# Optimization experiments

Hardware: AMD Instinct MI355X
Metric: run time of the kernel (lower is better)

The kernel has to match this reference:

```python
import jax, jax.numpy as jnp
import numpy as np

N_NODES = 100000
N_EDGES = 1600000
HID = 128
HEADS = 8
DK = HID // HEADS
N_LAYERS = 4
IN_DIM = 32
N_CLASSES = 16


def _ln(x, g, b, eps=1e-5):
    mu = x.mean(-1, keepdims=True)
    var = x.var(-1, keepdims=True)
    return (x - mu) / jnp.sqrt(var + eps) * g + b


def setup_inputs() -> dict:
    key = jax.random.key(0)
    ks = jax.random.split(key, 24)
    s = 0.05
    inp = {
        'feat': jax.random.randint(ks[0], (N_NODES,), 0, IN_DIM, dtype=jnp.int32),
        'edge_src': jax.random.randint(ks[1], (N_EDGES,), 0, N_NODES, dtype=jnp.int32),
        'edge_dst': jnp.sort(jax.random.randint(ks[2], (N_EDGES,), 0, N_NODES, dtype=jnp.int32)),
        'emb': jax.random.normal(ks[3], (IN_DIM, HID), jnp.float32) * s,
        'Wq': jax.random.normal(ks[4], (N_LAYERS, HID, HID), jnp.float32) * s,
        'Wk': jax.random.normal(ks[5], (N_LAYERS, HID, HID), jnp.float32) * s,
        'Wv': jax.random.normal(ks[6], (N_LAYERS, HID, HID), jnp.float32) * s,
        'Wo': jax.random.normal(ks[7], (N_LAYERS, HID, HID), jnp.float32) * s,
        'bo': jnp.zeros((N_LAYERS, HID), jnp.float32),
        'ln1_g': jnp.ones((N_LAYERS, HID), jnp.float32),
        'ln1_b': jnp.zeros((N_LAYERS, HID), jnp.float32),
        'W1': jax.random.normal(ks[8], (N_LAYERS, HID, 2 * HID), jnp.float32) * s,
        'b1': jnp.zeros((N_LAYERS, 2 * HID), jnp.float32),
        'W2': jax.random.normal(ks[9], (N_LAYERS, 2 * HID, HID), jnp.float32) * s,
        'b2': jnp.zeros((N_LAYERS, HID), jnp.float32),
        'ln2_g': jnp.ones((N_LAYERS, HID), jnp.float32),
        'ln2_b': jnp.zeros((N_LAYERS, HID), jnp.float32),
        'mW0': jax.random.normal(ks[10], (HID, HID // 2), jnp.float32) * s,
        'mb0': jnp.zeros((HID // 2,), jnp.float32),
        'mW1': jax.random.normal(ks[11], (HID // 2, HID // 4), jnp.float32) * s,
        'mb1': jnp.zeros((HID // 4,), jnp.float32),
        'mW2': jax.random.normal(ks[12], (HID // 4, N_CLASSES), jnp.float32) * s,
        'mb2': jnp.zeros((N_CLASSES,), jnp.float32),
    }
    return inp


def reference(feat, edge_src, edge_dst, emb, Wq, Wk, Wv, Wo, bo, ln1_g, ln1_b,
              W1, b1, W2, b2, ln2_g, ln2_b, mW0, mb0, mW1, mb1, mW2, mb2):
    N = feat.shape[0]
    h = emb[feat]  # [N, HID] embedding gather
    inv_sqrt_dk = jnp.float32(1.0 / np.sqrt(DK))
    for l in range(Wq.shape[0]):
        h_in1 = h
        q = (h @ Wq[l]).reshape(N, HEADS, DK)
        k = (h @ Wk[l]).reshape(N, HEADS, DK)
        v = (h @ Wv[l]).reshape(N, HEADS, DK)
        # per-edge scores: K[src] . Q[dst], scaled, clipped, exponentiated
        sc = jnp.einsum('ehd,ehd->eh', k[edge_src], q[edge_dst]) * inv_sqrt_dk
        sc = jnp.exp(jnp.clip(sc, -5.0, 5.0))  # [E, HEADS]
        wV = jax.ops.segment_sum(sc[:, :, None] * v[edge_src], edge_dst, num_segments=N)
        z = jax.ops.segment_sum(sc, edge_dst, num_segments=N)
        attn = (wV / (z[:, :, None] + 1e-6)).reshape(N, HID)
        h = h_in1 + (attn @ Wo[l] + bo[l])  # residual + O proj
        h = _ln(h, ln1_g[l], ln1_b[l])
        h_in2 = h
        f = jax.nn.relu(h @ W1[l] + b1[l]) @ W2[l] + b2[l]
        h = _ln(h_in2 + f, ln2_g[l], ln2_b[l])
    # MLPReadout: HID -> HID/2 -> HID/4 -> n_classes
    h = jax.nn.relu(h @ mW0 + mb0)
    h = jax.nn.relu(h @ mW1 + mb1)
    return h @ mW2 + mb2
```

## Files before the change

### kernel.cpp

```cpp
#include <hip/hip_runtime.h>
#include <hip/hip_fp16.h>

#define HID 128
#define N_LAYERS 4
#define IN_DIM 32
#define N_CLASSES 16

typedef _Float16 f16x8 __attribute__((ext_vector_type(8)));
typedef _Float16 half2_t __attribute__((ext_vector_type(2)));
typedef float f32x2 __attribute__((ext_vector_type(2)));
typedef __attribute__((ext_vector_type(4))) float f32x4;
typedef unsigned int uint_t;

#if defined(__has_builtin)
#if __has_builtin(__builtin_amdgcn_cvt_pk_f32_fp8)
#define HAVE_CVT_FP8 1
#endif
#if __has_builtin(__builtin_amdgcn_cvt_pk_fp8_f32)
#define HAVE_ENC_FP8 1
#endif
#endif

__device__ __forceinline__ unsigned short f2bf(float f) {
    unsigned int u = __float_as_uint(f);
    return (unsigned short)((u + 0x7FFFu + ((u >> 16) & 1u)) >> 16);
}
__device__ __forceinline__ float2 up16(uint_t u) {
    __half2 h = *(__half2*)&u;
    return __half22float2(h);
}

__device__ __forceinline__ unsigned char f2e4m3(float f) {
    unsigned int u = __float_as_uint(f);
    unsigned char s = (unsigned char)((u >> 24) & 0x80u);
    unsigned int a = u & 0x7FFFFFFFu;
    if (a >= 0x43E00000u) return s | 0x7Eu;
    int exp = (int)(a >> 23) - 127;
    if (exp < -6) {
        int m = (int)rintf(__uint_as_float(a) * 512.f);
        return s | (unsigned char)m;
    }
    unsigned int lsb = (a >> 20) & 1u;
    a += 0x7FFFFu + lsb;
    int e8 = ((int)(a >> 23) - 127) + 7;
    unsigned int m8 = (a >> 20) & 7u;
    return s | (unsigned char)((e8 << 3) | (int)m8);
}
__device__ __forceinline__ float e4m32f(unsigned int b) {
    unsigned int s = (b & 0x80u) << 24;
    unsigned int E = (b >> 3) & 15u, m = b & 7u;
    if (E == 0) {
        float v = (float)m * 0.001953125f;
        return __uint_as_float(__float_as_uint(v) | s);
    }
    return __uint_as_float(s | ((E + 120u) << 23) | (m << 20));
}
__device__ __forceinline__ unsigned char enc8(float v) {
#ifdef HAVE_ENC_FP8
    int r = __builtin_amdgcn_cvt_pk_fp8_f32(v, v, 0, false);
    return (unsigned char)(r & 0xFF);
#else
    return f2e4m3(v);
#endif
}
__device__ __forceinline__ void dec8v(uint_t u, f32x2* o) {
#ifdef HAVE_CVT_FP8
    o[0] = __builtin_amdgcn_cvt_pk_f32_fp8(u, false);
    o[1] = __builtin_amdgcn_cvt_pk_f32_fp8(u, true);
#else
    o[0] = (f32x2){e4m32f(u & 255u), e4m32f((u >> 8) & 255u)};
    o[1] = (f32x2){e4m32f((u >> 16) & 255u), e4m32f(u >> 24)};
#endif
}

__global__ void detect_kernel(const unsigned int* __restrict__ ln1g, int* __restrict__ flag) {
    if (threadIdx.x == 0 && blockIdx.x == 0)
        *flag = (ln1g[0] == 0x3F800000u) ? 0 : 1;
}

#define NSM 11
struct SArgs {
    const void* src[NSM];
    float*      dst[NSM];
    int         cnt[NSM];
};

__global__ void conv_kernel(SArgs args, const int* __restrict__ flag) {
    int p = blockIdx.y;
    int n = args.cnt[p];
    int base = (blockIdx.x * 256 + threadIdx.x) * 4;
    if (base >= n) return;
    float* dst = args.dst[p];
    if (*flag) {
        const unsigned short* s = (const unsigned short*)args.src[p];
        #pragma unroll
        for (int j = 0; j < 4; ++j)
            dst[base + j] = __uint_as_float(((unsigned int)s[base + j]) << 16);
    } else {
        const float* s = (const float*)args.src[p];
        *(float4*)&dst[base] = *(const float4*)&s[base];
    }
}

#define NW 27
struct WArgs {
    const void* src[NW];
    int         soff[NW];
    _Float16*   dst[NW];
    int         K[NW];
    int         M[NW];
};

__global__ void wconv_kernel(WArgs a, const int* __restrict__ flag) {
    int p = blockIdx.y;
    int K = a.K[p], M = a.M[p];
    int idx = blockIdx.x * 256 + threadIdx.x;
    if (idx >= K * M) return;
    int k = idx / M, m = idx % M;
    float v;
    if (*flag)
        v = __uint_as_float(((unsigned int)((const unsigned short*)a.src[p])[a.soff[p] + idx]) << 16);
    else
        v = ((const float*)a.src[p])[a.soff[p] + idx];
    a.dst[p][(size_t)m * K + k] = (_Float16)v;
}

__global__ void csr_kernel(const int* __restrict__ dst, int* __restrict__ row_start,
                           int N, int E) {
    int n = blockIdx.x * 256 + threadIdx.x;
    if (n > N) return;
    int lo = 0, hi = E;
    while (lo < hi) {
        int mid = (lo + hi) >> 1;
        if (dst[mid] < n) lo = mid + 1; else hi = mid;
    }
    row_start[n] = lo;
}

__global__ void embed_kernel(const int* __restrict__ feat, const float* __restrict__ emb,
                             _Float16* __restrict__ h, int N) {
    int idx = blockIdx.x * 256 + threadIdx.x;
    if (idx >= N * 16) return;
    int n  = idx >> 4;
    int c8 = idx & 15;
    int f = feat[n];
    const float* s = &emb[(size_t)f * HID + c8 * 8];
    float4 a = *(const float4*)s;
    float4 b = *(const float4*)(s + 4);
    f16x8 o;
    o[0] = (_Float16)a.x; o[1] = (_Float16)a.y; o[2] = (_Float16)a.z; o[3] = (_Float16)a.w;
    o[4] = (_Float16)b.x; o[5] = (_Float16)b.y; o[6] = (_Float16)b.z; o[7] = (_Float16)b.w;
    *(f16x8*)&h[(size_t)n * HID + c8 * 8] = o;
}

template<int K, int KC, int MC, int MTOT, bool RELU, bool BIAS, int OUTMODE>
__launch_bounds__(256)
__global__ void mfma_gemm(const _Float16* __restrict__ Ain,
                          const _Float16* __restrict__ Bt,
                          const float* __restrict__ bias,
                          float* __restrict__ Cf, _Float16* __restrict__ C16,
                          _Float16* __restrict__ q16, unsigned char* __restrict__ kvp8,
                          void* __restrict__ outp, const int* __restrict__ flag, int Nrow) {
    constexpr int NT  = MC / 16;
    constexpr int SAB = KC * 2 + 16;
    constexpr int KNC = K / KC;

    __shared__ __align__(16) char As[64 * SAB];
    __shared__ __align__(16) char Bs[MC * SAB];

    const int t    = threadIdx.x;
    const int w    = t >> 6;
    const int l    = t & 63;
    const int quad = l >> 4;
    const int lc   = l & 15;
    const int row0 = blockIdx.x * 64;
    const int mbase = blockIdx.y * MC;

    f32x4 acc[NT];
    #pragma unroll
    for (int i = 0; i < NT; ++i) acc[i] = (f32x4){0.f, 0.f, 0.f, 0.f};

    for (int kc0 = 0; kc0 < K; kc0 += KC) {
        if (KNC > 1 && kc0 > 0) __syncthreads();
        constexpr int AU = 64 * KC / 8;
        #pragma unroll
        for (int i = 0; i < (AU + 255) / 256; ++i) {
            int idx = t + i * 256;
            if ((AU % 256 == 0) || idx < AU) {
                int r = idx / (KC / 8), u = idx % (KC / 8);
                *(uint4*)&As[r * SAB + u * 16] =
                    *(const uint4*)(Ain + (size_t)(row0 + r) * K + kc0 + u * 8);
            }
        }
        constexpr int BU = MC * KC / 8;
        #pragma unroll
        for (int i = 0; i < (BU + 255) / 256; ++i) {
            int idx = t + i * 256;
            if ((BU % 256 == 0) || idx < BU) {
                int m = idx / (KC / 8), u = idx % (KC / 8);
                *(uint4*)&Bs[m * SAB + u * 16] =
                    *(const uint4*)(Bt + (size_t)(mbase + m) * K + kc0 + u * 8);
            }
        }
        __syncthreads();
        #pragma unroll
        for (int kk = 0; kk < KC / 32; ++kk) {
            f16x8 af = *(const f16x8*)&As[(w * 16 + lc) * SAB + kk * 64 + quad * 16];
            #pragma unroll
            for (int i = 0; i < NT; ++i) {
                f16x8 bf = *(const f16x8*)&Bs[(i * 16 + lc) * SAB + kk * 64 + quad * 16];
                acc[i] = __builtin_amdgcn_mfma_f32_16x16x32_f16(af, bf, acc[i], 0, 0, 0);
            }
        }
    }

    if (BIAS) {
        #pragma unroll
        for (int i = 0; i < NT; ++i) {
            float bv = bias[mbase + i * 16 + lc];
            #pragma unroll
            for (int r = 0; r < 4; ++r) acc[i][r] += bv;
        }
    }
    #pragma unroll
    for (int r = 0; r < 4; ++r) {
        int row = row0 + w * 16 + quad * 4 + r;
        #pragma unroll
        for (int i = 0; i < NT; ++i) {
            float v = acc[i][r];
            if (RELU) v = fmaxf(v, 0.f);
            if (OUTMODE == 0) {
                Cf[(size_t)row * MTOT + mbase + i * 16 + lc] = v;
            } else if (OUTMODE == 1) {
                C16[(size_t)row * MTOT + mbase + i * 16 + lc] = (_Float16)v;
            } else if (OUTMODE == 2) {
                int gc = mbase + i * 16 + lc;
                if (gc < 128)      q16[(size_t)row * 128 + gc] = (_Float16)v;
                else if (gc < 256) kvp8[(size_t)row * 256 + (gc - 128)] = enc8(v);
                else               kvp8[(size_t)row * 256 + 128 + (gc - 256)] = enc8(v);
            } else {
                if (row < Nrow) {
                    size_t o = (size_t)row * MTOT + mbase + i * 16 + lc;
                    if (*flag) ((unsigned short*)outp)[o] = f2bf(v);
                    else       ((float*)outp)[o] = v;
                }
            }
        }
    }
}

__launch_bounds__(256)
__global__ void layer_tail(const _Float16* __restrict__ t2, _Float16* __restrict__ h,
                           const _Float16* __restrict__ Wo, const _Float16* __restrict__ W1,
                           const _Float16* __restrict__ W2,
                           const float* __restrict__ bo,  const float* __restrict__ l1g,
                           const float* __restrict__ l1b, const float* __restrict__ b1,
                           const float* __restrict__ b2,  const float* __restrict__ l2g,
                           const float* __restrict__ l2b) {
    constexpr int SAB = 272;
    __shared__ __align__(16) char bufA[64 * SAB];
    __shared__ __align__(16) char bufT[64 * SAB];
    __shared__ __align__(16) char bufH[64 * SAB];
    __shared__ __align__(16) char bufB[64 * SAB];

    const int t    = threadIdx.x;
    const int w    = t >> 6;
    const int l    = t & 63;
    const int quad = l >> 4;
    const int lc   = l & 15;
    const int row0 = blockIdx.x * 64;
    const int arow = (w * 16 + lc) * SAB;

    #pragma unroll
    for (int i = 0; i < 4; ++i) {
        int idx = t + i * 256;
        int r = idx >> 4, u = idx & 15;
        *(uint4*)&bufA[r * SAB + u * 16] = *(const uint4*)(t2 + (size_t)(row0 + r) * 128 + u * 8);
        *(uint4*)&bufT[r * SAB + u * 16] = *(const uint4*)(h  + (size_t)(row0 + r) * 128 + u * 8);
    }

    f32x4 acc[8];
    #pragma unroll
    for (int i = 0; i < 8; ++i) acc[i] = (f32x4){0.f, 0.f, 0.f, 0.f};
    #pragma unroll
    for (int c = 0; c < 2; ++c) {
        if (c) __syncthreads();
        #pragma unroll
        for (int i = 0; i < 4; ++i) {
            int idx = t + i * 256;
            int r = idx >> 4, u = idx & 15;
            *(uint4*)&bufB[r * SAB + u * 16] = *(const uint4*)(Wo + (size_t)(c * 64 + r) * 128 + u * 8);
        }
        __syncthreads();
        #pragma unroll
        for (int kk = 0; kk < 4; ++kk) {
            f16x8 af = *(const f16x8*)&bufA[arow + kk * 64 + quad * 16];
            #pragma unroll
            for (int i = 0; i < 4; ++i) {
                f16x8 bf = *(const f16x8*)&bufB[(i * 16 + lc) * SAB + kk * 64 + quad * 16];
                acc[c * 4 + i] = __builtin_amdgcn_mfma_f32_16x16x32_f16(af, bf, acc[c * 4 + i], 0, 0, 0);
            }
        }
    }
    {
        float gv[8], bv[8], bb[8];
        #pragma unroll
        for (int j = 0; j < 8; ++j) {
            int col = j * 16 + lc;
            gv[j] = l1g[col]; bv[j] = l1b[col]; bb[j] = bo[col];
        }
        #pragma unroll
        for (int r = 0; r < 4; ++r) {
            int lrow = (w * 16 + quad * 4 + r) * SAB;
            float v[8];
            float s = 0.f, ss = 0.f;
            #pragma unroll
            for (int j = 0; j < 8; ++j) {
                float res = (float)*(const _Float16*)&bufT[lrow + (j * 16 + lc) * 2];
                v[j] = acc[j][r] + bb[j] + res;
                s += v[j]; ss += v[j] * v[j];
            }
            #pragma unroll
            for (int m = 1; m <= 8; m <<= 1) { s += __shfl_xor(s, m); ss += __shfl_xor(ss, m); }
            float mu   = s * (1.f / 128.f);
            float rstd = rsqrtf(ss * (1.f / 128.f) - mu * mu + 1e-5f);
            #pragma unroll
            for (int j = 0; j < 8; ++j) {
                float o = (v[j] - mu) * rstd * gv[j] + bv[j];
                *(_Float16*)&bufH[lrow + (j * 16 + lc) * 2] = (_Float16)o;
            }
        }
    }

    #pragma unroll
    for (int c = 0; c < 4; ++c) {
        __syncthreads();
        #pragma unroll
        for (int i = 0; i < 4; ++i) {
            int idx = t + i * 256;
            int r = idx >> 4, u = idx & 15;
            *(uint4*)&bufB[r * SAB + u * 16] = *(const uint4*)(W1 + (size_t)(c * 64 + r) * 128 + u * 8);
        }
        __syncthreads();
        f32x4 a2[4];
        #pragma unroll
        for (int i = 0; i < 4; ++i) a2[i] = (f32x4){0.f, 0.f, 0.f, 0.f};
        #pragma unroll
        for (int kk = 0; kk < 4; ++kk) {
            f16x8 af = *(const f16x8*)&bufH[arow + kk * 64 + quad * 16];
            #pragma unroll
            for (int i = 0; i < 4; ++i) {
                f16x8 bf = *(const f16x8*)&bufB[(i * 16 + lc) * SAB + kk * 64 + quad * 16];
                a2[i] = __builtin_amdgcn_mfma_f32_16x16x32_f16(af, bf, a2[i], 0, 0, 0);
            }
        }
        char* plane = (c < 2) ? bufA : bufT;
        const int cbyte = (c & 1) * 128;
        #pragma unroll
        for (int r = 0; r < 4; ++r) {
            int lrow = (w * 16 + quad * 4 + r) * SAB;
            #pragma unroll
            for (int i = 0; i < 4; ++i) {
                float v = a2[i][r] + b1[c * 64 + i * 16 + lc];
                v = fmaxf(v, 0.f);
                *(_Float16*)&plane[lrow + cbyte + (i * 16 + lc) * 2] = (_Float16)v;
            }
        }
    }

    f32x4 acc3[8];
    #pragma unroll
    for (int i = 0; i < 8; ++i) acc3[i] = (f32x4){0.f, 0.f, 0.f, 0.f};
    #pragma unroll
    for (int cc = 0; cc < 2; ++cc) {
        #pragma unroll
        for (int kh = 0; kh < 2; ++kh) {
            __syncthreads();
            #pragma unroll
            for (int i = 0; i < 4; ++i) {
                int idx = t + i * 256;
                int r = idx >> 4, u = idx & 15;
                *(uint4*)&bufB[r * SAB + u * 16] =
                    *(const uint4*)(W2 + (size_t)(cc * 64 + r) * 256 + kh * 128 + u * 8);
            }
            __syncthreads();
            const char* Ap = kh ? bufT : bufA;
            #pragma unroll
            for (int kk = 0; kk < 4; ++kk) {
                f16x8 af = *(const f16x8*)&Ap[arow + kk * 64 + quad * 16];
                #pragma unroll
                for (int i = 0; i < 4; ++i) {
                    f16x8 bf = *(const f16x8*)&bufB[(i * 16 + lc) * SAB + kk * 64 + quad * 16];
                    acc3[cc * 4 + i] = __builtin_amdgcn_mfma_f32_16x16x32_f16(af, bf, acc3[cc * 4 + i], 0, 0, 0);
                }
            }
        }
    }
    {
        float gv[8], bv[8], bb[8];
        #pragma unroll
        for (int j = 0; j < 8; ++j) {
            int col = j * 16 + lc;
            gv[j] = l2g[col]; bv[j] = l2b[col]; bb[j] = b2[col];
        }
        #pragma unroll
        for (int r = 0; r < 4; ++r) {
            int row = row0 + w * 16 + quad * 4 + r;
            int lrow = (w * 16 + quad * 4 + r) * SAB;
            float v[8];
            float s = 0.f, ss = 0.f;
            #pragma unroll
            for (int j = 0; j < 8; ++j) {
                float res = (float)*(const _Float16*)&bufH[lrow + (j * 16 + lc) * 2];
                v[j] = acc3[j][r] + bb[j] + res;
                s += v[j]; ss += v[j] * v[j];
            }
            #pragma unroll
            for (int m = 1; m <= 8; m <<= 1) { s += __shfl_xor(s, m); ss += __shfl_xor(ss, m); }
            float mu   = s * (1.f / 128.f);
            float rstd = rsqrtf(ss * (1.f / 128.f) - mu * mu + 1e-5f);
            #pragma unroll
            for (int j = 0; j < 8; ++j) {
                float o = (v[j] - mu) * rstd * gv[j] + bv[j];
                h[(size_t)row * 128 + j * 16 + lc] = (_Float16)o;
            }
        }
    }
}

__global__ void attn_kernel(const _Float16* __restrict__ q16, const uint_t* __restrict__ kvp,
                            const int* __restrict__ esrc, const int* __restrict__ rows,
                            _Float16* __restrict__ out, int N) {
    int node = (blockIdx.x * blockDim.x + threadIdx.x) >> 6;
    if (node >= N) return;
    int l    = threadIdx.x & 63;
    int head = l & 7;
    int eg   = l >> 3;

    f32x2 qh[8];
    {
        const uint4* qp = (const uint4*)(q16 + (size_t)node * HID + head * 16);
        uint4 q0 = qp[0], q1 = qp[1];
        uint_t qs[8] = {q0.x, q0.y, q0.z, q0.w, q1.x, q1.y, q1.z, q1.w};
        #pragma unroll
        for (int i = 0; i < 8; ++i) {
            float2 f = up16(qs[i]);
            qh[i] = (f32x2){f.x * 0.25f, f.y * 0.25f};
        }
    }
    int e0 = rows[node], e1 = rows[node + 1];
    f32x2 wv[8];
    #pragma unroll
    for (int i = 0; i < 8; ++i) wv[i] = (f32x2){0.f, 0.f};
    float z = 0.f;

    for (int eb = e0; eb < e1; eb += 16) {
        int ea = eb + eg, ec = eb + 8 + eg;
        bool oka = ea < e1, okc = ec < e1;
        int sa  = esrc[oka ? ea : e1 - 1];
        int sc_ = esrc[okc ? ec : e1 - 1];
        uint4 ka = *(const uint4*)(kvp + (size_t)sa  * 64 + head * 4);
        uint4 va = *(const uint4*)(kvp + (size_t)sa  * 64 + 32 + head * 4);
        uint4 kc = *(const uint4*)(kvp + (size_t)sc_ * 64 + head * 4);
        uint4 vc = *(const uint4*)(kvp + (size_t)sc_ * 64 + 32 + head * 4);

        f32x2 k2a[8], k2c[8];
        dec8v(ka.x, k2a); dec8v(ka.y, k2a + 2); dec8v(ka.z, k2a + 4); dec8v(ka.w, k2a + 6);
        dec8v(kc.x, k2c); dec8v(kc.y, k2c + 2); dec8v(kc.z, k2c + 4); dec8v(kc.w, k2c + 6);
        f32x2 da2 = (f32x2){0.f, 0.f}, dc2 = (f32x2){0.f, 0.f};
        #pragma unroll
        for (int j = 0; j < 8; ++j) { da2 += qh[j] * k2a[j]; dc2 += qh[j] * k2c[j]; }
        float da = da2.x + da2.y, dc = dc2.x + dc2.y;
        float sa2 = oka ? __expf(fminf(fmaxf(da, -5.f), 5.f)) : 0.f;
        float sc2 = okc ? __expf(fminf(fmaxf(dc, -5.f), 5.f)) : 0.f;

        f32x2 v2a[8], v2c[8];
        dec8v(va.x, v2a); dec8v(va.y, v2a + 2); dec8v(va.z, v2a + 4); dec8v(va.w, v2a + 6);
        dec8v(vc.x, v2c); dec8v(vc.y, v2c + 2); dec8v(vc.z, v2c + 4); dec8v(vc.w, v2c + 6);
        f32x2 pa = (f32x2){sa2, sa2}, pc = (f32x2){sc2, sc2};
        #pragma unroll
        for (int j = 0; j < 8; ++j) { wv[j] += pa * v2a[j]; wv[j] += pc * v2c[j]; }
        z += sa2 + sc2;
    }
    #pragma unroll
    for (int m = 8; m < 64; m <<= 1) {
        z += __shfl_xor(z, m);
        #pragma unroll
        for (int i = 0; i < 8; ++i) {
            wv[i].x += __shfl_xor(wv[i].x, m);
            wv[i].y += __shfl_xor(wv[i].y, m);
        }
    }
    if (eg == 0) {
        float inv = 1.f / (z + 1e-6f);
        f16x8 o0, o1;
        #pragma unroll
        for (int i = 0; i < 4; ++i) {
            o0[2*i]   = (_Float16)(wv[i].x * inv);
            o0[2*i+1] = (_Float16)(wv[i].y * inv);
            o1[2*i]   = (_Float16)(wv[4+i].x * inv);
            o1[2*i+1] = (_Float16)(wv[4+i].y * inv);
        }
        *(f16x8*)&out[(size_t)node * HID + head * 16]     = o0;
        *(f16x8*)&out[(size_t)node * HID + head * 16 + 8] = o1;
    }
}

extern "C" void kernel_launch(void* const* d_in, const int* in_sizes, int n_in,
                              void* d_out, int out_size, void* d_ws, size_t ws_size,
                              hipStream_t stream) {
    const int N  = in_sizes[0];
    const int E  = in_sizes[1];
    const int RB = (N + 63) / 64;
    const size_t NP = (size_t)RB * 64;

    const int* d_feat = (const int*)d_in[0];
    const int* d_esrc = (const int*)d_in[1];
    const int* d_edst = (const int*)d_in[2];

    char* base = (char*)d_ws;
    size_t cur = 0;
    auto alloc = [&](size_t bytes) -> char* {
        cur = (cur + 255) & ~(size_t)255;
        char* p = base + cur;
        cur += bytes;
        return p;
    };
    int* d_flag = (int*)alloc(4);
    int* d_rows = (int*)alloc((size_t)(N + 1) * 4);

    float* p_emb = (float*)alloc(IN_DIM * HID * 4);
    float* p_bo  = (float*)alloc(N_LAYERS * HID * 4);
    float* p_l1g = (float*)alloc(N_LAYERS * HID * 4);
    float* p_l1b = (float*)alloc(N_LAYERS * HID * 4);
    float* p_b1  = (float*)alloc(N_LAYERS * 2 * HID * 4);
    float* p_b2  = (float*)alloc(N_LAYERS * HID * 4);
    float* p_l2g = (float*)alloc(N_LAYERS * HID * 4);
    float* p_l2b = (float*)alloc(N_LAYERS * HID * 4);
    float* p_mb0 = (float*)alloc(64 * 4);
    float* p_mb1 = (float*)alloc(32 * 4);
    float* p_mb2 = (float*)alloc(16 * 4);

    _Float16* wqkv_t = (_Float16*)alloc((size_t)N_LAYERS * 384 * 128 * 2);
    _Float16* wo_t   = (_Float16*)alloc((size_t)N_LAYERS * 128 * 128 * 2);
    _Float16* w1_t   = (_Float16*)alloc((size_t)N_LAYERS * 256 * 128 * 2);
    _Float16* w2_t   = (_Float16*)alloc((size_t)N_LAYERS * 128 * 256 * 2);
    _Float16* mw0_t  = (_Float16*)alloc(64 * 128 * 2);
    _Float16* mw1_t  = (_Float16*)alloc(32 * 64 * 2);
    _Float16* mw2_t  = (_Float16*)alloc(16 * 32 * 2);

    _Float16*      buf_h = (_Float16*)alloc(NP * HID * 2);
    _Float16*      q16   = (_Float16*)alloc(NP * HID * 2);
    _Float16*      t2    = (_Float16*)alloc(NP * HID * 2);
    unsigned char* kvp   = (unsigned char*)alloc(NP * 256);

    detect_kernel<<<1, 64, 0, stream>>>((const unsigned int*)d_in[9], d_flag);

    {
        SArgs sa;
        const int sidx[NSM] = {3, 8, 9, 10, 12, 14, 15, 16, 18, 20, 22};
        float*    sdst[NSM] = {p_emb, p_bo, p_l1g, p_l1b, p_b1, p_b2, p_l2g, p_l2b, p_mb0, p_mb1, p_mb2};
        const int scnt[NSM] = {IN_DIM*HID, N_LAYERS*HID, N_LAYERS*HID, N_LAYERS*HID,
                               N_LAYERS*2*HID, N_LAYERS*HID, N_LAYERS*HID, N_LAYERS*HID, 64, 32, 16};
        for (int i = 0; i < NSM; ++i) { sa.src[i] = d_in[sidx[i]]; sa.dst[i] = sdst[i]; sa.cnt[i] = scnt[i]; }
        conv_kernel<<<dim3(4, NSM), 256, 0, stream>>>(sa, d_flag);
    }

    {
        WArgs wa;
        int wi = 0;
        auto addw = [&](int inp, int off, int Kd, int Md, _Float16* dst) {
            wa.src[wi] = d_in[inp]; wa.soff[wi] = off; wa.K[wi] = Kd; wa.M[wi] = Md;
            wa.dst[wi] = dst; ++wi;
        };
        for (int l = 0; l < N_LAYERS; ++l) {
            addw(4,  l * 16384, 128, 128, wqkv_t + (size_t)l * 49152);
            addw(5,  l * 16384, 128, 128, wqkv_t + (size_t)l * 49152 + 16384);
            addw(6,  l * 16384, 128, 128, wqkv_t + (size_t)l * 49152 + 32768);
            addw(7,  l * 16384, 128, 128, wo_t + (size_t)l * 16384);
            addw(11, l * 32768, 128, 256, w1_t + (size_t)l * 32768);
            addw(13, l * 32768, 256, 128, w2_t + (size_t)l * 32768);
        }
        addw(17, 0, 128, 64, mw0_t);
        addw(19, 0, 64,  32, mw1_t);
        addw(21, 0, 32,  16, mw2_t);
        wconv_kernel<<<dim3(128, NW), 256, 0, stream>>>(wa, d_flag);
    }

    csr_kernel<<<(N + 1 + 255) / 256, 256, 0, stream>>>(d_edst, d_rows, N, E);
    embed_kernel<<<((size_t)N * 16 + 255) / 256, 256, 0, stream>>>(d_feat, p_emb, buf_h, N);

    const int GBW = (N + 3) / 4;

    for (int l = 0; l < N_LAYERS; ++l) {
        const _Float16* Wqkv = wqkv_t + (size_t)l * 49152;
        const _Float16* Wo   = wo_t + (size_t)l * 16384;
        const _Float16* W1   = w1_t + (size_t)l * 32768;
        const _Float16* W2   = w2_t + (size_t)l * 32768;

        mfma_gemm<128, 128, 192, 384, false, false, 2>
            <<<dim3(RB, 2), 256, 0, stream>>>(buf_h, Wqkv, nullptr,
                                              nullptr, nullptr, q16, kvp, nullptr, nullptr, 0);
        attn_kernel<<<GBW, 256, 0, stream>>>(q16, (const uint_t*)kvp, d_esrc, d_rows, t2, N);
        layer_tail<<<RB, 256, 0, stream>>>(t2, buf_h, Wo, W1, W2,
                                           p_bo  + (size_t)l * HID,
                                           p_l1g + (size_t)l * HID,
                                           p_l1b + (size_t)l * HID,
                                           p_b1  + (size_t)l * 2 * HID,
                                           p_b2  + (size_t)l * HID,
                                           p_l2g + (size_t)l * HID,
                                           p_l2b + (size_t)l * HID);
    }

    mfma_gemm<128, 128, 64, 64, true, true, 1>
        <<<dim3(RB, 1), 256, 0, stream>>>(buf_h, mw0_t, p_mb0,
                                          nullptr, q16, nullptr, nullptr, nullptr, nullptr, 0);
    mfma_gemm<64, 64, 32, 32, true, true, 1>
        <<<dim3(RB, 1), 256, 0, stream>>>(q16, mw1_t, p_mb1,
                                          nullptr, t2, nullptr, nullptr, nullptr, nullptr, 0);
    mfma_gemm<32, 32, 16, 16, false, true, 3>
        <<<dim3(RB, 1), 256, 0, stream>>>(t2, mw2_t, p_mb2,
                                          nullptr, nullptr, nullptr, nullptr, d_out, d_flag, N);
}
```

Measured before the change: 859.2 us.

## Fuse next-layer QKV projection and readout GEMMs into layer tail kernel

The layer tail kernel now keeps the post-LayerNorm hidden tile in shared memory and immediately computes the next layer's QKV projection (or the first readout layer on the last layer), writing q16/kvp directly. The last two readout layers are merged into a single small kernel. This removes the separate QKV GEMM launches and one re-read of h per layer, plus two readout launches. In exchange the tail kernel does more serial work per block and loads extra weight tiles, which may lower occupancy.

```diff
diff --git a/kernel.cpp b/kernel.cpp
--- a/kernel.cpp
+++ b/kernel.cpp
@@ -7,7 +7,6 @@
 #define N_CLASSES 16
 
 typedef _Float16 f16x8 __attribute__((ext_vector_type(8)));
-typedef _Float16 half2_t __attribute__((ext_vector_type(2)));
 typedef float f32x2 __attribute__((ext_vector_type(2)));
 typedef __attribute__((ext_vector_type(4))) float f32x4;
 typedef unsigned int uint_t;
@@ -153,17 +152,13 @@
     *(f16x8*)&h[(size_t)n * HID + c8 * 8] = o;
 }
 
-template<int K, int KC, int MC, int MTOT, bool RELU, bool BIAS, int OUTMODE>
+template<int K, int KC, int MC>
 __launch_bounds__(256)
-__global__ void mfma_gemm(const _Float16* __restrict__ Ain,
-                          const _Float16* __restrict__ Bt,
-                          const float* __restrict__ bias,
-                          float* __restrict__ Cf, _Float16* __restrict__ C16,
-                          _Float16* __restrict__ q16, unsigned char* __restrict__ kvp8,
-                          void* __restrict__ outp, const int* __restrict__ flag, int Nrow) {
+__global__ void mfma_gemm_qkv(const _Float16* __restrict__ Ain,
+                              const _Float16* __restrict__ Bt,
+                              _Float16* __restrict__ q16, unsigned char* __restrict__ kvp8) {
     constexpr int NT  = MC / 16;
     constexpr int SAB = KC * 2 + 16;
-    constexpr int KNC = K / KC;
 
     __shared__ __align__(16) char As[64 * SAB];
     __shared__ __align__(16) char Bs[MC * SAB];
@@ -180,8 +175,7 @@
     #pragma unroll
     for (int i = 0; i < NT; ++i) acc[i] = (f32x4){0.f, 0.f, 0.f, 0.f};
 
-    for (int kc0 = 0; kc0 < K; kc0 += KC) {
-        if (KNC > 1 && kc0 > 0) __syncthreads();
+    {
         constexpr int AU = 64 * KC / 8;
         #pragma unroll
         for (int i = 0; i < (AU + 255) / 256; ++i) {
@@ -189,7 +183,7 @@
             if ((AU % 256 == 0) || idx < AU) {
                 int r = idx / (KC / 8), u = idx % (KC / 8);
                 *(uint4*)&As[r * SAB + u * 16] =
-                    *(const uint4*)(Ain + (size_t)(row0 + r) * K + kc0 + u * 8);
+                    *(const uint4*)(Ain + (size_t)(row0 + r) * K + u * 8);
             }
         }
         constexpr int BU = MC * KC / 8;
@@ -199,7 +193,7 @@
             if ((BU % 256 == 0) || idx < BU) {
                 int m = idx / (KC / 8), u = idx % (KC / 8);
                 *(uint4*)&Bs[m * SAB + u * 16] =
-                    *(const uint4*)(Bt + (size_t)(mbase + m) * K + kc0 + u * 8);
+                    *(const uint4*)(Bt + (size_t)(mbase + m) * K + u * 8);
             }
         }
         __syncthreads();
@@ -214,49 +208,31 @@
         }
     }
 
-    if (BIAS) {
-        #pragma unroll
-        for (int i = 0; i < NT; ++i) {
-            float bv = bias[mbase + i * 16 + lc];
-            #pragma unroll
-            for (int r = 0; r < 4; ++r) acc[i][r] += bv;
-        }
-    }
     #pragma unroll
     for (int r = 0; r < 4; ++r) {
         int row = row0 + w * 16 + quad * 4 + r;
         #pragma unroll
         for (int i = 0; i < NT; ++i) {
             float v = acc[i][r];
-            if (RELU) v = fmaxf(v, 0.f);
-            if (OUTMODE == 0) {
-                Cf[(size_t)row * MTOT + mbase + i * 16 + lc] = v;
-            } else if (OUTMODE == 1) {
-                C16[(size_t)row * MTOT + mbase + i * 16 + lc] = (_Float16)v;
-            } else if (OUTMODE == 2) {
-                int gc = mbase + i * 16 + lc;
-                if (gc < 128)      q16[(size_t)row * 128 + gc] = (_Float16)v;
-                else if (gc < 256) kvp8[(size_t)row * 256 + (gc - 128)] = enc8(v);
-                else               kvp8[(size_t)row * 256 + 128 + (gc - 256)] = enc8(v);
-            } else {
-                if (row < Nrow) {
-                    size_t o = (size_t)row * MTOT + mbase + i * 16 + lc;
-                    if (*flag) ((unsigned short*)outp)[o] = f2bf(v);
-                    else       ((float*)outp)[o] = v;
-                }
-            }
-        }
-    }
-}
-
+            int gc = mbase + i * 16 + lc;
+            if (gc < 128)      q16[(size_t)row * 128 + gc] = (_Float16)v;
+            else if (gc < 256) kvp8[(size_t)row * 256 + (gc - 128)] = enc8(v);
+            else               kvp8[(size_t)row * 256 + 128 + (gc - 256)] = enc8(v);
+        }
+    }
+}
+
+template<int NEXTM, bool RMODE>
 __launch_bounds__(256)
-__global__ void layer_tail(const _Float16* __restrict__ t2, _Float16* __restrict__ h,
-                           const _Float16* __restrict__ Wo, const _Float16* __restrict__ W1,
-                           const _Float16* __restrict__ W2,
-                           const float* __restrict__ bo,  const float* __restrict__ l1g,
-                           const float* __restrict__ l1b, const float* __restrict__ b1,
-                           const float* __restrict__ b2,  const float* __restrict__ l2g,
-                           const float* __restrict__ l2b) {
+__global__ void layer_tail_fused(const _Float16* __restrict__ t2, _Float16* __restrict__ h,
+                                 const _Float16* __restrict__ Wo, const _Float16* __restrict__ W1,
+                                 const _Float16* __restrict__ W2,
+                                 const _Float16* __restrict__ Wn, const float* __restrict__ bn,
+                                 const float* __restrict__ bo,  const float* __restrict__ l1g,
+                                 const float* __restrict__ l1b, const float* __restrict__ b1,
+                                 const float* __restrict__ b2,  const float* __restrict__ l2g,
+                                 const float* __restrict__ l2b,
+                                 _Float16* __restrict__ q16, unsigned char* __restrict__ kvp8) {
     constexpr int SAB = 272;
     __shared__ __align__(16) char bufA[64 * SAB];
     __shared__ __align__(16) char bufT[64 * SAB];
@@ -423,7 +399,115 @@
             for (int j = 0; j < 8; ++j) {
                 float o = (v[j] - mu) * rstd * gv[j] + bv[j];
                 h[(size_t)row * 128 + j * 16 + lc] = (_Float16)o;
-            }
+                *(_Float16*)&bufA[lrow + (j * 16 + lc) * 2] = (_Float16)o;
+            }
+        }
+    }
+
+    #pragma unroll
+    for (int c = 0; c < NEXTM / 64; ++c) {
+        __syncthreads();
+        #pragma unroll
+        for (int i = 0; i < 4; ++i) {
+            int idx = t + i * 256;
+            int r = idx >> 4, u = idx & 15;
+            *(uint4*)&bufB[r * SAB + u * 16] = *(const uint4*)(Wn + (size_t)(c * 64 + r) * 128 + u * 8);
+        }
+        __syncthreads();
+        f32x4 a4[4];
+        #pragma unroll
+        for (int i = 0; i < 4; ++i) a4[i] = (f32x4){0.f, 0.f, 0.f, 0.f};
+        #pragma unroll
+        for (int kk = 0; kk < 4; ++kk) {
+            f16x8 af = *(const f16x8*)&bufA[arow + kk * 64 + quad * 16];
+            #pragma unroll
+            for (int i = 0; i < 4; ++i) {
+                f16x8 bf = *(const f16x8*)&bufB[(i * 16 + lc) * SAB + kk * 64 + quad * 16];
+                a4[i] = __builtin_amdgcn_mfma_f32_16x16x32_f16(af, bf, a4[i], 0, 0, 0);
+            }
+        }
+        #pragma unroll
+        for (int r = 0; r < 4; ++r) {
+            int row = row0 + w * 16 + quad * 4 + r;
+            #pragma unroll
+            for (int i = 0; i < 4; ++i) {
+                int gc = c * 64 + i * 16 + lc;
+                float v = a4[i][r];
+                if (RMODE) {
+                    v += bn[gc];
+                    v = fmaxf(v, 0.f);
+                    q16[(size_t)row * 64 + gc] = (_Float16)v;
+                } else {
+                    if (gc < 128)      q16[(size_t)row * 128 + gc] = (_Float16)v;
+                    else if (gc < 256) kvp8[(size_t)row * 256 + (gc - 128)] = enc8(v);
+                    else               kvp8[(size_t)row * 256 + 128 + (gc - 256)] = enc8(v);
+                }
+            }
+        }
+    }
+}
+
+__launch_bounds__(256)
+__global__ void readout_tail(const _Float16* __restrict__ r0,
+                             const _Float16* __restrict__ w1t, const float* __restrict__ b1_,
+                             const _Float16* __restrict__ w2t, const float* __restrict__ b2_,
+                             void* __restrict__ outp, const int* __restrict__ flag, int N) {
+    constexpr int SA = 144;
+    constexpr int SR = 80;
+    __shared__ __align__(16) char bufA[64 * SA];
+    __shared__ __align__(16) char bufR[64 * SR];
+
+    const int t    = threadIdx.x;
+    const int w    = t >> 6;
+    const int l    = t & 63;
+    const int quad = l >> 4;
+    const int lc   = l & 15;
+    const int row0 = blockIdx.x * 64;
+
+    #pragma unroll
+    for (int i = 0; i < 2; ++i) {
+        int idx = t + i * 256;
+        int r = idx >> 3, u = idx & 7;
+        *(uint4*)&bufA[r * SA + u * 16] = *(const uint4*)(r0 + (size_t)(row0 + r) * 64 + u * 8);
+    }
+    __syncthreads();
+
+    f32x4 acc[2];
+    acc[0] = (f32x4){0.f, 0.f, 0.f, 0.f};
+    acc[1] = (f32x4){0.f, 0.f, 0.f, 0.f};
+    #pragma unroll
+    for (int kk = 0; kk < 2; ++kk) {
+        f16x8 af = *(const f16x8*)&bufA[(w * 16 + lc) * SA + kk * 64 + quad * 16];
+        #pragma unroll
+        for (int i = 0; i < 2; ++i) {
+            f16x8 bf = *(const f16x8*)(w1t + (size_t)(i * 16 + lc) * 64 + kk * 32 + quad * 8);
+            acc[i] = __builtin_amdgcn_mfma_f32_16x16x32_f16(af, bf, acc[i], 0, 0, 0);
+        }
+    }
+    #pragma unroll
+    for (int r = 0; r < 4; ++r) {
+        int lrow = (w * 16 + quad * 4 + r) * SR;
+        #pragma unroll
+        for (int i = 0; i < 2; ++i) {
+            float v = acc[i][r] + b1_[i * 16 + lc];
+            v = fmaxf(v, 0.f);
+            *(_Float16*)&bufR[lrow + (i * 16 + lc) * 2] = (_Float16)v;
+        }
+    }
+    f32x4 a2 = (f32x4){0.f, 0.f, 0.f, 0.f};
+    {
+        f16x8 af = *(const f16x8*)&bufR[(w * 16 + lc) * SR + quad * 16];
+        f16x8 bf = *(const f16x8*)(w2t + (size_t)lc * 32 + quad * 8);
+        a2 = __builtin_amdgcn_mfma_f32_16x16x32_f16(af, bf, a2, 0, 0, 0);
+    }
+    #pragma unroll
+    for (int r = 0; r < 4; ++r) {
+        int row = row0 + w * 16 + quad * 4 + r;
+        if (row < N) {
+            float v = a2[r] + b2_[lc];
+            size_t o = (size_t)row * 16 + lc;
+            if (*flag) ((unsigned short*)outp)[o] = f2bf(v);
+            else       ((float*)outp)[o] = v;
         }
     }
 }
@@ -592,33 +676,32 @@
 
     const int GBW = (N + 3) / 4;
 
+    mfma_gemm_qkv<128, 128, 192><<<dim3(RB, 2), 256, 0, stream>>>(buf_h, wqkv_t, q16, kvp);
+
     for (int l = 0; l < N_LAYERS; ++l) {
-        const _Float16* Wqkv = wqkv_t + (size_t)l * 49152;
-        const _Float16* Wo   = wo_t + (size_t)l * 16384;
-        const _Float16* W1   = w1_t + (size_t)l * 32768;
-        const _Float16* W2   = w2_t + (size_t)l * 32768;
-
-        mfma_gemm<128, 128, 192, 384, false, false, 2>
-            <<<dim3(RB, 2), 256, 0, stream>>>(buf_h, Wqkv, nullptr,
-                                              nullptr, nullptr, q16, kvp, nullptr, nullptr, 0);
+        const _Float16* Wo = wo_t + (size_t)l * 16384;
+        const _Float16* W1 = w1_t + (size_t)l * 32768;
+        const _Float16* W2 = w2_t + (size_t)l * 32768;
+        const float* bo  = p_bo  + (size_t)l * HID;
+        const float* l1g = p_l1g + (size_t)l * HID;
+        const float* l1b = p_l1b + (size_t)l * HID;
+        const float* b1  = p_b1  + (size_t)l * 2 * HID;
+        const float* b2  = p_b2  + (size_t)l * HID;
+        const float* l2g = p_l2g + (size_t)l * HID;
+        const float* l2b = p_l2b + (size_t)l * HID;
+
         attn_kernel<<<GBW, 256, 0, stream>>>(q16, (const uint_t*)kvp, d_esrc, d_rows, t2, N);
-        layer_tail<<<RB, 256, 0, stream>>>(t2, buf_h, Wo, W1, W2,
-                                           p_bo  + (size_t)l * HID,
-                                           p_l1g + (size_t)l * HID,
-                                           p_l1b + (size_t)l * HID,
-                                           p_b1  + (size_t)l * 2 * HID,
-                                           p_b2  + (size_t)l * HID,
-                                           p_l2g + (size_t)l * HID,
-                                           p_l2b + (size_t)l * HID);
-    }
-
-    mfma_gemm<128, 128, 64, 64, true, true, 1>
-        <<<dim3(RB, 1), 256, 0, stream>>>(buf_h, mw0_t, p_mb0,
-                                          nullptr, q16, nullptr, nullptr, nullptr, nullptr, 0);
-    mfma_gemm<64, 64, 32, 32, true, true, 1>
-        <<<dim3(RB, 1), 256, 0, stream>>>(q16, mw1_t, p_mb1,
-                                          nullptr, t2, nullptr, nullptr, nullptr, nullptr, 0);
-    mfma_gemm<32, 32, 16, 16, false, true, 3>
-        <<<dim3(RB, 1), 256, 0, stream>>>(t2, mw2_t, p_mb2,
-                                          nullptr, nullptr, nullptr, nullptr, d_out, d_flag, N);
-}
+
+        if (l < N_LAYERS - 1) {
+            layer_tail_fused<384, false><<<RB, 256, 0, stream>>>(
+                t2, buf_h, Wo, W1, W2, wqkv_t + (size_t)(l + 1) * 49152, nullptr,
+                bo, l1g, l1b, b1, b2, l2g, l2b, q16, kvp);
+        } else {
+            layer_tail_fused<64, true><<<RB, 256, 0, stream>>>(
+                t2, buf_h, Wo, W1, W2, mw0_t, p_mb0,
+                bo, l1g, l1b, b1, b2, l2g, l2b, q16, nullptr);
+        }
+    }
+
+    readout_tail<<<RB, 256, 0, stream>>>(q16, mw1_t, p_mb1, mw2_t, p_mb2, d_out, d_flag, N);
+}
```

Measured after the change: 842.6 us. About the same (-1.9%).
